# Optimization experiments

Hardware: AMD Instinct MI355X
Metric: run time of the kernel (lower is better)

The kernel has to match this reference:

```python
import jax, jax.numpy as jnp
import numpy as np

N, E, F_IN = 50000, 1_600_000, 256
HID, HEADS, NCLS = 8, 8, 16  # conv1: 8 heads x 8 dims (concat=64); conv2: 1 head -> 16 classes


def setup_inputs() -> dict:
    key = jax.random.key(0)
    ks = jax.random.split(key, 11)
    x = jax.random.normal(ks[0], (N, F_IN), dtype=jnp.float32)
    edge_index = jax.random.randint(ks[1], (2, E), 0, N, dtype=jnp.int32)
    s1 = 1.0 / np.sqrt(F_IN)
    W1 = jax.random.normal(ks[2], (F_IN, HEADS * HID), jnp.float32) * s1
    a_src1 = jax.random.normal(ks[3], (HEADS, HID), jnp.float32) * 0.1
    a_dst1 = jax.random.normal(ks[4], (HEADS, HID), jnp.float32) * 0.1
    b1 = jnp.zeros((HEADS * HID,), jnp.float32)
    s2 = 1.0 / np.sqrt(HEADS * HID)
    W2 = jax.random.normal(ks[5], (HEADS * HID, NCLS), jnp.float32) * s2
    a_src2 = jax.random.normal(ks[6], (1, NCLS), jnp.float32) * 0.1
    a_dst2 = jax.random.normal(ks[7], (1, NCLS), jnp.float32) * 0.1
    b2 = jnp.zeros((NCLS,), jnp.float32)
    return {"x": x, "edge_index": edge_index, "W1": W1, "a_src1": a_src1,
            "a_dst1": a_dst1, "b1": b1, "W2": W2, "a_src2": a_src2,
            "a_dst2": a_dst2, "b2": b2}


def _gat_conv(x, W, a_src, a_dst, bias, src, dst, n, heads, ch, concat):
    # per-head linear transform: [n, heads, ch]
    h = (x @ W).reshape(n, heads, ch)
    # additive attention logits per node, per head
    al_s = jnp.einsum('nhc,hc->nh', h, a_src)
    al_d = jnp.einsum('nhc,hc->nh', h, a_dst)
    e = jax.nn.leaky_relu(al_s[src] + al_d[dst], 0.2)  # [E_tot, heads]
    # segment softmax grouped by destination node (self-loops guarantee non-empty segments)
    m = jax.ops.segment_max(e, dst, num_segments=n)
    ex = jnp.exp(e - m[dst])
    den = jax.ops.segment_sum(ex, dst, num_segments=n)
    alpha = ex / den[dst]  # [E_tot, heads]
    # scatter-aggregate weighted neighbor features
    out = jax.ops.segment_sum(h[src] * alpha[:, :, None], dst, num_segments=n)
    out = out.reshape(n, heads * ch) if concat else out.mean(axis=1)
    return out + bias


def reference(x, edge_index, W1, a_src1, a_dst1, b1, W2, a_src2, a_dst2, b2):
    # add self-loops (PyG GATConv default)
    loops = jnp.arange(N, dtype=edge_index.dtype)
    src = jnp.concatenate([edge_index[0], loops])
    dst = jnp.concatenate([edge_index[1], loops])
    h = _gat_conv(x, W1, a_src1, a_dst1, b1, src, dst, N, HEADS, HID, True)
    h = jax.nn.elu(h)
    out = _gat_conv(h, W2, a_src2, a_dst2, b2, src, dst, N, 1, NCLS, False)
    return jax.nn.log_softmax(out, axis=1)
```

## Files before the change

kernel.cpp:

```cpp
#include <hip/hip_runtime.h>
#include <hip/hip_fp16.h>
#include <hip/hip_fp8.h>

#define NN   50000
#define FIN  256
#define C1   64
#define NH   8
#define NC   16
#define NE   1600000
#define NTOT (NE + NN)

#define CH   256
#define EPC  ((NTOT + CH - 1) / CH)
#define NCB  196
#define GB1  ((NN + 63) / 64)

typedef _Float16 half8 __attribute__((ext_vector_type(8)));
typedef _Float16 half4 __attribute__((ext_vector_type(4)));
typedef float f32x4 __attribute__((ext_vector_type(4)));
typedef float floatx2 __attribute__((ext_vector_type(2)));

#if __has_builtin(__builtin_amdgcn_cvt_pk_f32_fp8) && __has_builtin(__builtin_amdgcn_cvt_pk_fp8_f32)
#define FP8_FAST 1
#endif

__device__ __forceinline__ unsigned pack4_fp8(float f0, float f1, float f2, float f3) {
#ifdef FP8_FAST
    int d = 0;
    d = __builtin_amdgcn_cvt_pk_fp8_f32(f0, f1, d, false);
    d = __builtin_amdgcn_cvt_pk_fp8_f32(f2, f3, d, true);
    return (unsigned)d;
#else
    __hip_fp8_e4m3 q0(f0), q1(f1), q2(f2), q3(f3);
    return (unsigned)q0.__x | ((unsigned)q1.__x << 8) |
           ((unsigned)q2.__x << 16) | ((unsigned)q3.__x << 24);
#endif
}

__device__ __forceinline__ void cvt8_fp8_pk(unsigned lo, unsigned hi,
                                            floatx2* p0, floatx2* p1,
                                            floatx2* p2, floatx2* p3) {
#ifdef FP8_FAST
    *p0 = __builtin_amdgcn_cvt_pk_f32_fp8((int)lo, false);
    *p1 = __builtin_amdgcn_cvt_pk_f32_fp8((int)lo, true);
    *p2 = __builtin_amdgcn_cvt_pk_f32_fp8((int)hi, false);
    *p3 = __builtin_amdgcn_cvt_pk_f32_fp8((int)hi, true);
#else
    float f[8];
    #pragma unroll
    for (int u = 0; u < 4; ++u) {
        __hip_fp8_e4m3 q; q.__x = (unsigned char)((lo >> (8*u)) & 0xff);
        f[u] = (float)q;
        __hip_fp8_e4m3 p; p.__x = (unsigned char)((hi >> (8*u)) & 0xff);
        f[4+u] = (float)p;
    }
    (*p0)[0]=f[0]; (*p0)[1]=f[1]; (*p1)[0]=f[2]; (*p1)[1]=f[3];
    (*p2)[0]=f[4]; (*p2)[1]=f[5]; (*p3)[0]=f[6]; (*p3)[1]=f[7];
#endif
}

#define OFF_H1F8  0
#define OFF_ALS1H 800000
#define OFF_G1H   1600000
#define OFF_STAGE 3200000
#define OFF_H2H   3200000
#define OFF_ALS2  3600000
#define OFF_ALD2  3650000
#define OFF_ALD1  6800000
#define OFF_HM    7200000
#define OFF_BASEK 7300352
#define OFF_BTOT  7400704
#define OFF_OFFS  7401600
#define OFF_SRC   7451700

__global__ __launch_bounds__(256) void k_g1rh(const float* __restrict__ x,
                                              const float* __restrict__ W1,
                                              const float* __restrict__ as1,
                                              const float* __restrict__ ad1,
                                              unsigned char* __restrict__ h1f8,
                                              _Float16* __restrict__ als1h,
                                              float* __restrict__ ald,
                                              const int* __restrict__ ei,
                                              int* __restrict__ H) {
    __shared__ _Float16 wsT[64][264];
    __shared__ int lh[NCB];
    const int tid = threadIdx.x;

    if (blockIdx.x >= GB1) {
        int k = blockIdx.x - GB1;
        for (int i = tid; i < NCB; i += 256) lh[i] = 0;
        __syncthreads();
        int e0 = k * EPC, e1 = min(e0 + EPC, NTOT);
        for (int e = e0 + tid; e < e1; e += 256) {
            int d = (e < NE) ? ei[NE + e] : (e - NE);
            atomicAdd(&lh[d >> 8], 1);
        }
        __syncthreads();
        for (int i = tid; i < NCB; i += 256) H[k * NCB + i] = lh[i];
        return;
    }

    const int r0 = blockIdx.x * 64;
    {
        int c = tid & 63, kb = tid >> 6;
        #pragma unroll
        for (int j = 0; j < 8; ++j) {
            int k8 = kb + 4 * j;
            half8 hv;
            #pragma unroll
            for (int u = 0; u < 8; ++u)
                hv[u] = (_Float16)W1[(size_t)(k8 * 8 + u) * C1 + c];
            *(half8*)(&wsT[c][k8 * 8]) = hv;
        }
    }
    __syncthreads();

    const int lane = tid & 63;
    const int wv   = tid >> 6;
    const int colb = lane & 15;
    const int rgrp = lane >> 4;
    const int arow = r0 + wv * 16 + colb;
    const bool arv = arow < NN;
    f32x4 acc[4] = {};
    #pragma unroll
    for (int s = 0; s < 8; ++s) {
        float4 v0 = make_float4(0.f,0.f,0.f,0.f), v1 = v0;
        if (arv) {
            const float4* xp = (const float4*)(&x[(size_t)arow * FIN + s * 32 + rgrp * 8]);
            v0 = xp[0]; v1 = xp[1];
        }
        half8 a;
        a[0]=(_Float16)v0.x; a[1]=(_Float16)v0.y; a[2]=(_Float16)v0.z; a[3]=(_Float16)v0.w;
        a[4]=(_Float16)v1.x; a[5]=(_Float16)v1.y; a[6]=(_Float16)v1.z; a[7]=(_Float16)v1.w;
        #pragma unroll
        for (int ct = 0; ct < 4; ++ct) {
            half8 b = *(half8*)(&wsT[ct * 16 + colb][s * 32 + rgrp * 8]);
            acc[ct] = __builtin_amdgcn_mfma_f32_16x16x32_f16(a, b, acc[ct], 0, 0, 0);
        }
    }
    __syncthreads();
    _Float16 (*hstore)[72] = (_Float16(*)[72])wsT;
    #pragma unroll
    for (int j = 0; j < 4; ++j) {
        int row = wv * 16 + rgrp * 4 + j;
        #pragma unroll
        for (int ct = 0; ct < 4; ++ct)
            hstore[row][ct * 16 + colb] = (_Float16)acc[ct][j];
    }
    __syncthreads();
    {
        int row = tid >> 2, seg = tid & 3;
        int grow = r0 + row;
        if (grow < NN) {
            half8 h0 = *(half8*)(&hstore[row][seg * 16]);
            half8 h1v = *(half8*)(&hstore[row][seg * 16 + 8]);
            float fv[16];
            #pragma unroll
            for (int u = 0; u < 8; ++u) { fv[u] = (float)h0[u]; fv[8 + u] = (float)h1v[u]; }
            uint4 pk;
            pk.x = pack4_fp8(fv[0],  fv[1],  fv[2],  fv[3]);
            pk.y = pack4_fp8(fv[4],  fv[5],  fv[6],  fv[7]);
            pk.z = pack4_fp8(fv[8],  fv[9],  fv[10], fv[11]);
            pk.w = pack4_fp8(fv[12], fv[13], fv[14], fv[15]);
            *(uint4*)(&h1f8[(size_t)grow * 64 + seg * 16]) = pk;
            float ps0 = 0.f, pd0 = 0.f, ps1 = 0.f, pd1 = 0.f;
            #pragma unroll
            for (int u = 0; u < 8; ++u) {
                ps0 += fv[u]     * as1[seg * 16 + u];
                pd0 += fv[u]     * ad1[seg * 16 + u];
                ps1 += fv[8 + u] * as1[seg * 16 + 8 + u];
                pd1 += fv[8 + u] * ad1[seg * 16 + 8 + u];
            }
            als1h[grow * NH + seg * 2]     = (_Float16)ps0;
            als1h[grow * NH + seg * 2 + 1] = (_Float16)ps1;
            ald[grow * NH + seg * 2]     = pd0;
            ald[grow * NH + seg * 2 + 1] = pd1;
        }
    }
}

__global__ __launch_bounds__(256) void k_rsA(const int* __restrict__ H,
                                             int* __restrict__ basek,
                                             int* __restrict__ btot) {
    __shared__ int sc[CH];
    int b = blockIdx.x, t = threadIdx.x;
    int v = H[t * NCB + b];
    sc[t] = v;
    __syncthreads();
    for (int s = 1; s < CH; s <<= 1) {
        int u = (t >= s) ? sc[t - s] : 0;
        __syncthreads();
        sc[t] += u;
        __syncthreads();
    }
    basek[b * CH + t] = sc[t] - v;
    if (t == CH - 1) btot[b] = sc[t];
}

__global__ __launch_bounds__(256) void k_rscatter(const int* __restrict__ ei,
                                                  const int* __restrict__ basek,
                                                  const int* __restrict__ btot,
                                                  int* __restrict__ stage) {
    __shared__ int sc[256];
    __shared__ int lcur[NCB];
    int k = blockIdx.x, t = threadIdx.x;
    int v = (t < NCB) ? btot[t] : 0;
    sc[t] = v;
    __syncthreads();
    for (int s = 1; s < 256; s <<= 1) {
        int u = (t >= s) ? sc[t - s] : 0;
        __syncthreads();
        sc[t] += u;
        __syncthreads();
    }
    if (t < NCB) lcur[t] = (sc[t] - v) + basek[t * CH + k];
    __syncthreads();
    int e0 = k * EPC, e1 = min(e0 + EPC, NTOT);
    for (int e = e0 + t; e < e1; e += 256) {
        int s, d;
        if (e < NE) { s = ei[e]; d = ei[NE + e]; }
        else        { s = e - NE; d = s; }
        int pos = atomicAdd(&lcur[d >> 8], 1);
        stage[pos] = (s << 8) | (d & 255);
    }
}

__global__ __launch_bounds__(256) void k_fsort(const int* __restrict__ stage,
                                               const int* __restrict__ btot,
                                               int* __restrict__ offs,
                                               int* __restrict__ ssrc) {
    __shared__ int sc[256];
    __shared__ int lc[256];
    __shared__ int ls[256];
    __shared__ int lcur[256];
    __shared__ int bb[2];
    int b = blockIdx.x, t = threadIdx.x;
    int v = (t < NCB) ? btot[t] : 0;
    sc[t] = v;
    __syncthreads();
    for (int s = 1; s < 256; s <<= 1) {
        int u = (t >= s) ? sc[t - s] : 0;
        __syncthreads();
        sc[t] += u;
        __syncthreads();
    }
    if (t == b) bb[0] = sc[t] - v;
    if (t == b) bb[1] = sc[t];
    if (b == 0 && t == 0) offs[NN] = NTOT;
    lc[t] = 0;
    __syncthreads();
    int base = bb[0];
    int n = bb[1] - base;
    const int* sp = &stage[base];
    for (int i = t; i < n; i += 256) atomicAdd(&lc[sp[i] & 255], 1);
    __syncthreads();
    int hv = lc[t];
    ls[t] = hv;
    __syncthreads();
    for (int s = 1; s < 256; s <<= 1) {
        int u = (t >= s) ? ls[t - s] : 0;
        __syncthreads();
        ls[t] += u;
        __syncthreads();
    }
    int excl = ls[t] - hv;
    int d = b * 256 + t;
    if (d < NN) offs[d] = base + excl;
    lcur[t] = base + excl;
    __syncthreads();
    for (int i = t; i < n; i += 256) {
        int u = sp[i];
        int pos = atomicAdd(&lcur[u & 255], 1);
        ssrc[pos] = u >> 8;
    }
}

__global__ __launch_bounds__(256) void k_agg1(const int* __restrict__ offs,
                                              const int* __restrict__ src,
                                              const unsigned char* __restrict__ h1f8,
                                              const _Float16* __restrict__ als1h,
                                              const float* __restrict__ ald,
                                              const float* __restrict__ b1,
                                              _Float16* __restrict__ g1h) {
    int d = blockIdx.x * 4 + (threadIdx.x >> 6);
    if (d >= NN) return;
    const int l = threadIdx.x & 63;
    const int slot = l >> 3, hd = l & 7;
    const unsigned coff = (unsigned)hd * 8u;
    int beg = offs[d], end = offs[d + 1];
    float aldv = ald[d * NH + hd];
    floatx2 acc2[4] = {};
    float wsum = 0.f;

    for (int r = beg; r < end; r += 16) {
        int e0 = r + slot, e1 = e0 + 8;
        bool v0 = e0 < end, v1 = e1 < end;
        int s0 = src[v0 ? e0 : end - 1];
        int s1 = src[v1 ? e1 : end - 1];
        uint2 q0 = *(const uint2*)(h1f8 + ((unsigned)s0 * 64u + coff));
        uint2 q1 = *(const uint2*)(h1f8 + ((unsigned)s1 * 64u + coff));
        float lg0 = (float)als1h[s0 * NH + hd] + aldv;
        float lg1 = (float)als1h[s1 * NH + hd] + aldv;
        lg0 = lg0 > 0.f ? lg0 : 0.2f * lg0;
        lg1 = lg1 > 0.f ? lg1 : 0.2f * lg1;
        float w0 = v0 ? __expf(lg0) : 0.f;
        float w1 = v1 ? __expf(lg1) : 0.f;
        wsum += w0 + w1;
        floatx2 a0, a1, a2, a3, c0, c1, c2, c3;
        cvt8_fp8_pk(q0.x, q0.y, &a0, &a1, &a2, &a3);
        cvt8_fp8_pk(q1.x, q1.y, &c0, &c1, &c2, &c3);
        floatx2 w0v = {w0, w0}, w1v = {w1, w1};
        acc2[0] += w0v * a0 + w1v * c0;
        acc2[1] += w0v * a1 + w1v * c1;
        acc2[2] += w0v * a2 + w1v * c2;
        acc2[3] += w0v * a3 + w1v * c3;
    }
    float acc[8];
    #pragma unroll
    for (int u = 0; u < 4; ++u) { acc[2*u] = acc2[u][0]; acc[2*u+1] = acc2[u][1]; }
    #pragma unroll
    for (int u = 0; u < 8; ++u) {
        acc[u] += __shfl_xor(acc[u], 8);
        acc[u] += __shfl_xor(acc[u], 16);
        acc[u] += __shfl_xor(acc[u], 32);
    }
    wsum += __shfl_xor(wsum, 8);
    wsum += __shfl_xor(wsum, 16);
    wsum += __shfl_xor(wsum, 32);
    if (slot == 0) {
        half8 gv;
        #pragma unroll
        for (int u = 0; u < 8; ++u) {
            float o = acc[u] / wsum + b1[hd * 8 + u];
            o = o > 0.f ? o : (__expf(o) - 1.f);
            gv[u] = (_Float16)o;
        }
        *(half8*)(&g1h[(size_t)d * C1 + hd * 8]) = gv;
    }
}

__global__ __launch_bounds__(256) void k_gemm2(const _Float16* __restrict__ g1h,
                                               const float* __restrict__ W2,
                                               const float* __restrict__ as2,
                                               const float* __restrict__ ad2,
                                               _Float16* __restrict__ h2h,
                                               float* __restrict__ als2,
                                               float* __restrict__ ald2) {
    __shared__ float w2s[C1][17];
    __shared__ _Float16 hact[16][C1 + 8];
    int tid = threadIdx.x;
    for (int i = tid; i < C1 * NC; i += 256) w2s[i >> 4][i & 15] = W2[i];
    int ln = tid >> 4, j = tid & 15;
    int n = blockIdx.x * 16 + ln;
    if (n < NN)
        *(half4*)(&hact[ln][j * 4]) = *(const half4*)(&g1h[(size_t)n * C1 + j * 4]);
    __syncthreads();
    if (n >= NN) return;
    float sum = 0.f;
    #pragma unroll
    for (int c = 0; c < C1; ++c) sum += (float)hact[ln][c] * w2s[c][j];
    h2h[(size_t)n * NC + j] = (_Float16)sum;
    float ps = sum * as2[j], pd = sum * ad2[j];
    #pragma unroll
    for (int w = 1; w < 16; w <<= 1) {
        ps += __shfl_xor(ps, w);
        pd += __shfl_xor(pd, w);
    }
    if (j == 0) { als2[n] = ps; ald2[n] = pd; }
}

__global__ __launch_bounds__(256) void k_agg2(const int* __restrict__ offs,
                                              const int* __restrict__ src,
                                              const _Float16* __restrict__ h2h,
                                              const float* __restrict__ als2,
                                              const float* __restrict__ ald2,
                                              const float* __restrict__ b2,
                                              float* __restrict__ out) {
    int d = blockIdx.x * 4 + (threadIdx.x >> 6);
    if (d >= NN) return;
    const int l = threadIdx.x & 63;
    const int slot = l >> 2, cq = l & 3;
    const unsigned coff = (unsigned)cq * 8u;
    const char* h2b = (const char*)h2h;
    const char* alb = (const char*)als2;
    int beg = offs[d], end = offs[d + 1];
    float aldv = ald2[d];
    float acc[4] = {};
    float wsum = 0.f;
    for (int r = beg; r < end; r += 16) {
        int e = r + slot;
        bool v = e < end;
        int s = src[v ? e : end - 1];
        half4 hv = *(const half4*)(h2b + ((unsigned)s * 32u + coff));
        float lg = *(const float*)(alb + (unsigned)s * 4u) + aldv;
        lg = lg > 0.f ? lg : 0.2f * lg;
        float w = v ? __expf(lg) : 0.f;
        wsum += w;
        #pragma unroll
        for (int u = 0; u < 4; ++u)
            acc[u] += w * (float)hv[u];
    }
    #pragma unroll
    for (int u = 0; u < 4; ++u) {
        acc[u] += __shfl_xor(acc[u], 4);
        acc[u] += __shfl_xor(acc[u], 8);
        acc[u] += __shfl_xor(acc[u], 16);
        acc[u] += __shfl_xor(acc[u], 32);
    }
    wsum += __shfl_xor(wsum, 4);
    wsum += __shfl_xor(wsum, 8);
    wsum += __shfl_xor(wsum, 16);
    wsum += __shfl_xor(wsum, 32);
    float o[4];
    float m = -1e30f;
    #pragma unroll
    for (int u = 0; u < 4; ++u) {
        o[u] = acc[u] / wsum + b2[cq * 4 + u];
        m = fmaxf(m, o[u]);
    }
    m = fmaxf(m, __shfl_xor(m, 1));
    m = fmaxf(m, __shfl_xor(m, 2));
    float sm = 0.f;
    #pragma unroll
    for (int u = 0; u < 4; ++u) sm += __expf(o[u] - m);
    sm += __shfl_xor(sm, 1);
    sm += __shfl_xor(sm, 2);
    float lse = m + __logf(sm);
    if (slot == 0) {
        float4 ov = make_float4(o[0] - lse, o[1] - lse, o[2] - lse, o[3] - lse);
        *(float4*)(&out[(size_t)d * NC + cq * 4]) = ov;
    }
}

extern "C" void kernel_launch(void* const* d_in, const int* in_sizes, int n_in,
                              void* d_out, int out_size, void* d_ws, size_t ws_size,
                              hipStream_t stream) {
    const float* x   = (const float*)d_in[0];
    const int*   ei  = (const int*)  d_in[1];
    const float* W1  = (const float*)d_in[2];
    const float* as1 = (const float*)d_in[3];
    const float* ad1 = (const float*)d_in[4];
    const float* b1  = (const float*)d_in[5];
    const float* W2  = (const float*)d_in[6];
    const float* as2 = (const float*)d_in[7];
    const float* ad2 = (const float*)d_in[8];
    const float* b2  = (const float*)d_in[9];
    float* ws  = (float*)d_ws;
    float* out = (float*)d_out;

    unsigned char* h1f8 = (unsigned char*)(ws + OFF_H1F8);
    _Float16*  als1h = (_Float16*)(ws + OFF_ALS1H);
    _Float16*  g1h  = (_Float16*)(ws + OFF_G1H);
    _Float16*  h2h  = (_Float16*)(ws + OFF_H2H);
    float* ald1 = ws + OFF_ALD1;
    float* als2 = ws + OFF_ALS2;
    float* ald2 = ws + OFF_ALD2;
    int* H      = (int*)(ws + OFF_HM);
    int* basek  = (int*)(ws + OFF_BASEK);
    int* btot   = (int*)(ws + OFF_BTOT);
    int* offs   = (int*)(ws + OFF_OFFS);
    int* ssrc   = (int*)(ws + OFF_SRC);
    int* stage  = (int*)(ws + OFF_STAGE);

    k_g1rh    <<<GB1 + CH,       256, 0, stream>>>(x, W1, as1, ad1, h1f8, als1h, ald1, ei, H);
    k_rsA     <<<NCB,            256, 0, stream>>>(H, basek, btot);
    k_rscatter<<<CH,             256, 0, stream>>>(ei, basek, btot, stage);
    k_fsort   <<<NCB,            256, 0, stream>>>(stage, btot, offs, ssrc);
    k_agg1    <<<(NN + 3) / 4,   256, 0, stream>>>(offs, ssrc, h1f8, als1h, ald1, b1, g1h);
    k_gemm2   <<<(NN + 15) / 16, 256, 0, stream>>>(g1h, W2, as2, ad2, h2h, als2, ald2);
    k_agg2    <<<(NN + 3) / 4,   256, 0, stream>>>(offs, ssrc, h2h, als2, ald2, b2, out);
}
```

Before: 132.7 us.

## Fold bucket-prefix scan kernel into scatter and fine-sort kernels

```diff
diff --git a/kernel.cpp b/kernel.cpp
--- a/kernel.cpp
+++ b/kernel.cpp
@@ -68,8 +68,6 @@
 #define OFF_ALD2  3650000
 #define OFF_ALD1  6800000
 #define OFF_HM    7200000
-#define OFF_BASEK 7300352
-#define OFF_BTOT  7400704
 #define OFF_OFFS  7401600
 #define OFF_SRC   7451700
 
@@ -179,33 +177,21 @@
     }
 }
 
-__global__ __launch_bounds__(256) void k_rsA(const int* __restrict__ H,
-                                             int* __restrict__ basek,
-                                             int* __restrict__ btot) {
-    __shared__ int sc[CH];
-    int b = blockIdx.x, t = threadIdx.x;
-    int v = H[t * NCB + b];
-    sc[t] = v;
-    __syncthreads();
-    for (int s = 1; s < CH; s <<= 1) {
-        int u = (t >= s) ? sc[t - s] : 0;
-        __syncthreads();
-        sc[t] += u;
-        __syncthreads();
-    }
-    basek[b * CH + t] = sc[t] - v;
-    if (t == CH - 1) btot[b] = sc[t];
-}
-
 __global__ __launch_bounds__(256) void k_rscatter(const int* __restrict__ ei,
-                                                  const int* __restrict__ basek,
-                                                  const int* __restrict__ btot,
+                                                  const int* __restrict__ H,
                                                   int* __restrict__ stage) {
     __shared__ int sc[256];
     __shared__ int lcur[NCB];
     int k = blockIdx.x, t = threadIdx.x;
-    int v = (t < NCB) ? btot[t] : 0;
-    sc[t] = v;
+    int myTot = 0, myPre = 0;
+    if (t < NCB) {
+        for (int kk = 0; kk < CH; ++kk) {
+            int h = H[kk * NCB + t];
+            myTot += h;
+            if (kk < k) myPre += h;
+        }
+    }
+    sc[t] = (t < NCB) ? myTot : 0;
     __syncthreads();
     for (int s = 1; s < 256; s <<= 1) {
         int u = (t >= s) ? sc[t - s] : 0;
@@ -213,7 +199,7 @@
         sc[t] += u;
         __syncthreads();
     }
-    if (t < NCB) lcur[t] = (sc[t] - v) + basek[t * CH + k];
+    if (t < NCB) lcur[t] = (sc[t] - myTot) + myPre;
     __syncthreads();
     int e0 = k * EPC, e1 = min(e0 + EPC, NTOT);
     for (int e = e0 + t; e < e1; e += 256) {
@@ -226,7 +212,7 @@
 }
 
 __global__ __launch_bounds__(256) void k_fsort(const int* __restrict__ stage,
-                                               const int* __restrict__ btot,
+                                               const int* __restrict__ H,
                                                int* __restrict__ offs,
                                                int* __restrict__ ssrc) {
     __shared__ int sc[256];
@@ -235,8 +221,12 @@
     __shared__ int lcur[256];
     __shared__ int bb[2];
     int b = blockIdx.x, t = threadIdx.x;
-    int v = (t < NCB) ? btot[t] : 0;
-    sc[t] = v;
+    int myTot = 0;
+    if (t < NCB) {
+        for (int kk = 0; kk < CH; ++kk)
+            myTot += H[kk * NCB + t];
+    }
+    sc[t] = (t < NCB) ? myTot : 0;
     __syncthreads();
     for (int s = 1; s < 256; s <<= 1) {
         int u = (t >= s) ? sc[t - s] : 0;
@@ -244,8 +234,7 @@
         sc[t] += u;
         __syncthreads();
     }
-    if (t == b) bb[0] = sc[t] - v;
-    if (t == b) bb[1] = sc[t];
+    if (t == b) { bb[0] = sc[t] - myTot; bb[1] = sc[t]; }
     if (b == 0 && t == 0) offs[NN] = NTOT;
     lc[t] = 0;
     __syncthreads();
@@ -301,8 +290,8 @@
         uint2 q1 = *(const uint2*)(h1f8 + ((unsigned)s1 * 64u + coff));
         float lg0 = (float)als1h[s0 * NH + hd] + aldv;
         float lg1 = (float)als1h[s1 * NH + hd] + aldv;
-        lg0 = lg0 > 0.f ? lg0 : 0.2f * lg0;
-        lg1 = lg1 > 0.f ? lg1 : 0.2f * lg1;
+        lg0 = fmaxf(lg0, 0.2f * lg0);
+        lg1 = fmaxf(lg1, 0.2f * lg1);
         float w0 = v0 ? __expf(lg0) : 0.f;
         float w1 = v1 ? __expf(lg1) : 0.f;
         wsum += w0 + w1;
@@ -393,7 +382,7 @@
         int s = src[v ? e : end - 1];
         half4 hv = *(const half4*)(h2b + ((unsigned)s * 32u + coff));
         float lg = *(const float*)(alb + (unsigned)s * 4u) + aldv;
-        lg = lg > 0.f ? lg : 0.2f * lg;
+        lg = fmaxf(lg, 0.2f * lg);
         float w = v ? __expf(lg) : 0.f;
         wsum += w;
         #pragma unroll
@@ -456,16 +445,13 @@
     float* als2 = ws + OFF_ALS2;
     float* ald2 = ws + OFF_ALD2;
     int* H      = (int*)(ws + OFF_HM);
-    int* basek  = (int*)(ws + OFF_BASEK);
-    int* btot   = (int*)(ws + OFF_BTOT);
     int* offs   = (int*)(ws + OFF_OFFS);
     int* ssrc   = (int*)(ws + OFF_SRC);
     int* stage  = (int*)(ws + OFF_STAGE);
 
     k_g1rh    <<<GB1 + CH,       256, 0, stream>>>(x, W1, as1, ad1, h1f8, als1h, ald1, ei, H);
-    k_rsA     <<<NCB,            256, 0, stream>>>(H, basek, btot);
-    k_rscatter<<<CH,             256, 0, stream>>>(ei, basek, btot, stage);
-    k_fsort   <<<NCB,            256, 0, stream>>>(stage, btot, offs, ssrc);
+    k_rscatter<<<CH,             256, 0, stream>>>(ei, H, stage);
+    k_fsort   <<<NCB,            256, 0, stream>>>(stage, H, offs, ssrc);
     k_agg1    <<<(NN + 3) / 4,   256, 0, stream>>>(offs, ssrc, h1f8, als1h, ald1, b1, g1h);
     k_gemm2   <<<(NN + 15) / 16, 256, 0, stream>>>(g1h, W2, as2, ad2, h2h, als2, ald2);
     k_agg2    <<<(NN + 3) / 4,   256, 0, stream>>>(offs, ssrc, h2h, als2, ald2, b2, out);
```

New measurement: 145.9 us. +9.9%, slower.
